# Performance work log

Hardware: AMD Instinct MI355X
Metric: run time of the kernel (lower is better)

The kernel has to match this reference:

```python
import jax, jax.numpy as jnp
import numpy as np

B, N, C = 8, 6000, 21            # batch, proposals (pre_nms_topn), total_labels
VARIANCES = jnp.array([0.1, 0.1, 0.2, 0.2], jnp.float32)
MAX_TOTAL = 200                   # max_total_size == max_output_size_per_class
SCORE_THR = 0.5
IOU_THR = 0.5                     # tf combined_non_max_suppression default
NEG = -1e9                        # finite sentinel for suppressed scores


def setup_inputs() -> dict:
    key = jax.random.key(0)
    k1, k2, k3, k4 = jax.random.split(key, 4)
    # valid normalized rois: y1,x1 in [0,0.8), positive height/width
    yx1 = jax.random.uniform(k1, (B, N, 2), jnp.float32) * 0.8
    hw = jax.random.uniform(k4, (B, N, 2), jnp.float32) * 0.2 + 0.01
    roi_bboxes = jnp.concatenate([yx1, yx1 + hw], axis=-1)  # [B,N,4] y1x1y2x2
    pred_deltas = jax.random.normal(k2, (B, N, C * 4), jnp.float32) * 0.5
    pred_label_probs = jax.random.uniform(k3, (B, N, C), jnp.float32)
    return {"roi_bboxes": roi_bboxes, "pred_deltas": pred_deltas,
            "pred_label_probs": pred_label_probs}


def reference(roi_bboxes, pred_deltas, pred_label_probs):
    # --- bbox delta decoding ---
    deltas = pred_deltas.reshape(B, N, C, 4) * VARIANCES          # [B,N,C,4]
    roi = roi_bboxes[:, :, None, :]                               # [B,N,1,4]
    anc_h = roi[..., 2] - roi[..., 0]
    anc_w = roi[..., 3] - roi[..., 1]
    anc_cy = roi[..., 0] + 0.5 * anc_h
    anc_cx = roi[..., 1] + 0.5 * anc_w
    bh = jnp.exp(deltas[..., 2]) * anc_h
    bw = jnp.exp(deltas[..., 3]) * anc_w
    bcy = deltas[..., 0] * anc_h + anc_cy
    bcx = deltas[..., 1] * anc_w + anc_cx
    y1 = bcy - 0.5 * bh
    x1 = bcx - 0.5 * bw
    y2 = y1 + bh
    x2 = x1 + bw
    boxes = jnp.stack([y1, x1, y2, x2], axis=-1)                  # [B,N,C,4]
    boxes = jnp.clip(boxes, 0.0, 1.0)  # combined NMS clip_boxes=True default

    # zero out scores where argmax class is background (0)
    lbl = jnp.argmax(pred_label_probs, axis=-1)                   # [B,N]
    scores = jnp.where((lbl != 0)[..., None], pred_label_probs, 0.0)

    boxes = boxes.transpose(0, 2, 1, 3)                           # [B,C,N,4]
    scores = scores.transpose(0, 2, 1)                            # [B,C,N]
    s0 = jnp.where(scores > SCORE_THR, scores, NEG)

    areas = (jnp.maximum(boxes[..., 2] - boxes[..., 0], 0.0) *
             jnp.maximum(boxes[..., 3] - boxes[..., 1], 0.0))     # [B,C,N]

    # --- greedy per-class NMS, vectorized over (B,C) ---
    def step(s, _):
        idx = jnp.argmax(s, axis=-1)                              # [B,C]
        val = jnp.take_along_axis(s, idx[..., None], axis=-1)[..., 0]
        box = jnp.take_along_axis(boxes, idx[..., None, None], axis=2)[..., 0, :]
        valid = val > NEG * 0.5
        iy1 = jnp.maximum(box[..., None, 0], boxes[..., 0])
        ix1 = jnp.maximum(box[..., None, 1], boxes[..., 1])
        iy2 = jnp.minimum(box[..., None, 2], boxes[..., 2])
        ix2 = jnp.minimum(box[..., None, 3], boxes[..., 3])
        inter = jnp.maximum(iy2 - iy1, 0.0) * jnp.maximum(ix2 - ix1, 0.0)
        sel_a = (jnp.maximum(box[..., 2] - box[..., 0], 0.0) *
                 jnp.maximum(box[..., 3] - box[..., 1], 0.0))
        iou = inter / (sel_a[..., None] + areas - inter + 1e-8)   # [B,C,N]
        s = jnp.where((iou > IOU_THR) & valid[..., None], NEG, s)
        return s, (box, val, valid)

    _, (sel_box, sel_val, sel_ok) = jax.lax.scan(step, s0, None, length=MAX_TOTAL)
    # [T,B,C,*] -> [B, C*T, *]
    sel_box = sel_box.transpose(1, 2, 0, 3).reshape(B, C * MAX_TOTAL, 4)
    sel_val = sel_val.transpose(1, 2, 0).reshape(B, C * MAX_TOTAL)
    sel_ok = sel_ok.transpose(1, 2, 0).reshape(B, C * MAX_TOTAL)
    cls = jnp.broadcast_to(jnp.arange(C, dtype=jnp.float32)[None, :, None],
                           (B, C, MAX_TOTAL)).reshape(B, C * MAX_TOTAL)

    sel_val = jnp.where(sel_ok, sel_val, NEG)
    top_s, top_i = jax.lax.top_k(sel_val, MAX_TOTAL)              # [B,200]
    fb = jnp.take_along_axis(sel_box, top_i[..., None], axis=1)
    fc = jnp.take_along_axis(cls, top_i, axis=1)
    ok = top_s > NEG * 0.5
    final_scores = jnp.where(ok, top_s, 0.0)
    final_bboxes = jnp.where(ok[..., None], fb, 0.0)
    final_labels = jnp.where(ok, fc, 0.0)
    return final_bboxes, final_labels, final_scores
```

## Files before the change

### kernel.cpp

```cpp
#include <hip/hip_runtime.h>

#define B_    8
#define N_    6000
#define C_    21
#define MAXT  200
#define NEGV  -1000000000.0f
#define UCAP  4096
#define CCAP  1024
#define CTGT  512
#define NBUCK 64
#define NTH   1024
#define NENT  (C_ * MAXT)
#define NBLK  (B_ * C_)


__device__ __forceinline__ unsigned ford(float f) {
  unsigned u = __float_as_uint(f);
  return (u & 0x80000000u) ? ~u : (u | 0x80000000u);
}
__device__ __forceinline__ float funord(unsigned o) {
  unsigned u = (o & 0x80000000u) ? (o ^ 0x80000000u) : ~o;
  return __uint_as_float(u);
}

__device__ __forceinline__ float4 decode_box(const float* __restrict__ roi,
                                             const float* __restrict__ deltas,
                                             int b, int n, int c)
{
#pragma clang fp contract(off)
  float4 r = *(const float4*)(roi + ((size_t)b * N_ + n) * 4);
  float4 d = *(const float4*)(deltas + ((size_t)b * N_ + n) * (C_ * 4) + c * 4);
  float d0 = d.x * 0.1f, d1 = d.y * 0.1f, d2 = d.z * 0.2f, d3 = d.w * 0.2f;
  float ah = r.z - r.x, aw = r.w - r.y;
  float acy = r.x + 0.5f * ah, acx = r.y + 0.5f * aw;
  float bh = expf(d2) * ah, bw = expf(d3) * aw;
  float bcy = d0 * ah + acy, bcx = d1 * aw + acx;
  float y1 = bcy - 0.5f * bh, x1 = bcx - 0.5f * bw;
  float y2 = y1 + bh, x2 = x1 + bw;
  y1 = fminf(fmaxf(y1, 0.f), 1.f); x1 = fminf(fmaxf(x1, 0.f), 1.f);
  y2 = fminf(fmaxf(y2, 0.f), 1.f); x2 = fminf(fmaxf(x2, 0.f), 1.f);
  return make_float4(y1, x1, y2, x2);
}

__device__ __forceinline__ float iou_ref(float4 s, float4 o) {
#pragma clang fp contract(off)
  float iy1 = fmaxf(s.x, o.x), ix1 = fmaxf(s.y, o.y);
  float iy2 = fminf(s.z, o.z), ix2 = fminf(s.w, o.w);
  float inter = fmaxf(iy2 - iy1, 0.f) * fmaxf(ix2 - ix1, 0.f);
  float sa = fmaxf(s.z - s.x, 0.f) * fmaxf(s.w - s.y, 0.f);
  float oa = fmaxf(o.z - o.x, 0.f) * fmaxf(o.w - o.y, 0.f);
  return inter / (sa + oa - inter + 1e-08f);
}

struct Smem {
  unsigned long long ukeys[UCAP];
  unsigned long long cbuf[CCAP];
  float4 cboxAll[512];
  float4 comm[MAXT];
  unsigned long long kill[64];
  unsigned long long s_dead[16];
  int hist[NBUCK];
  int wcnt[16];
  int s_cnt, s_clen, s_ncomm, s_blo, s_len;
};

__global__ __launch_bounds__(256) void prep_kernel(
    const float* __restrict__ probs, float* __restrict__ probsT)
{
  int t = blockIdx.x * 256 + threadIdx.x;
  if (t >= B_ * N_) return;
  int b = t / N_, n = t - b * N_;
  const float* pr = probs + (size_t)t * C_;
  float p[C_];
  #pragma unroll
  for (int k = 0; k < C_; ++k) p[k] = pr[k];
  float mx = p[0]; int am = 0;
  #pragma unroll
  for (int k = 1; k < C_; ++k) { if (p[k] > mx) { mx = p[k]; am = k; } }
  float msk = (am != 0) ? 1.0f : 0.0f;
  #pragma unroll
  for (int c = 0; c < C_; ++c)
    probsT[((size_t)b * C_ + c) * N_ + n] = p[c] * msk;
}

__global__ __launch_bounds__(NTH) void nms_kernel(
    const float* __restrict__ roi, const float* __restrict__ deltas,
    const float* __restrict__ probs, const float* __restrict__ probsT,
    float* __restrict__ sel_val, float* __restrict__ sel_box)
{
#pragma clang fp contract(off)
  __shared__ Smem sm;
  const int bc = blockIdx.x, b = bc / C_, c = bc % C_;
  const int tid = threadIdx.x, lane = tid & 63, wv = tid >> 6;

  if (tid < NBUCK) sm.hist[tid] = 0;
  if (tid == 0) { sm.s_cnt = 0; sm.s_ncomm = 0; }
  __syncthreads();

  int M;
  const float* rowT = probsT ? (probsT + (size_t)bc * N_) : nullptr;
  if (rowT) {
    float scv[6];
    #pragma unroll
    for (int it = 0; it < 6; ++it) {
      int n = it * NTH + tid;
      scv[it] = (n < N_) ? rowT[n] : 0.f;
    }
    int off[6];
    int wtot = 0;
    #pragma unroll
    for (int it = 0; it < 6; ++it) {
      bool cand = (scv[it] > 0.5f);
      unsigned long long m = __ballot(cand);
      off[it] = wtot + __popcll(m & ((1ULL << lane) - 1ULL));
      wtot += __popcll(m);
    }
    if (lane == 0) sm.wcnt[wv] = wtot;
    __syncthreads();
    int wbase = 0, mtot = 0;
    #pragma unroll
    for (int w = 0; w < 16; ++w) {
      int t2 = sm.wcnt[w];
      if (w < wv) wbase += t2;
      mtot += t2;
    }
    #pragma unroll
    for (int it = 0; it < 6; ++it) {
      if (scv[it] > 0.5f) {
        int pos = wbase + off[it];
        if (pos < UCAP) {
          unsigned hi = ford(scv[it]);
          int n = it * NTH + tid;
          sm.ukeys[pos] = ((unsigned long long)hi << 32) |
                          (unsigned)(0xFFFFFFFFu - (unsigned)n);
          atomicAdd(&sm.hist[(hi >> 17) & (NBUCK - 1)], 1);
        }
      }
    }
    __syncthreads();
    M = mtot < UCAP ? mtot : UCAP;
  } else {
    for (int base0 = 0; base0 < N_; base0 += NTH) {
      int n = base0 + tid;
      bool cand = false;
      float sc = 0.f;
      if (n < N_) {
        const float* pr = probs + ((size_t)b * N_ + n) * C_;
        float mx = pr[0]; int am = 0;
        #pragma unroll
        for (int k = 1; k < C_; ++k) { float v = pr[k]; if (v > mx) { mx = v; am = k; } }
        if (am != 0) sc = pr[c];
        cand = (sc > 0.5f);
      }
      unsigned long long m = __ballot(cand);
      int wcnt2 = __popcll(m);
      int bslot = 0;
      if (lane == 0 && wcnt2) bslot = atomicAdd(&sm.s_cnt, wcnt2);
      bslot = __shfl(bslot, 0);
      if (cand) {
        int pos = bslot + __popcll(m & ((1ULL << lane) - 1ULL));
        if (pos < UCAP) {
          unsigned hi = ford(sc);
          sm.ukeys[pos] = ((unsigned long long)hi << 32) |
                          (unsigned)(0xFFFFFFFFu - (unsigned)n);
          atomicAdd(&sm.hist[(hi >> 17) & (NBUCK - 1)], 1);
        }
      }
    }
    __syncthreads();
    M = sm.s_cnt < UCAP ? sm.s_cnt : UCAP;
  }

  float* sv = sel_val + (size_t)bc * MAXT;
  float* sb = sel_box + (size_t)bc * MAXT * 4;

  int bhi = NBUCK - 1;
  while (true) {
    if (sm.s_ncomm >= MAXT || bhi < 0) break;

    if (wv == 0) {
      int h = (lane <= bhi) ? sm.hist[bhi - lane] : 0;
      int p = h;
      #pragma unroll
      for (int d = 1; d < 64; d <<= 1) {
        int o = __shfl_up(p, d);
        if (lane >= d) p += o;
      }
      unsigned long long ok = __ballot(p <= CTGT);
      int m = __popcll(ok);
      if (m == 0) m = 1;
      if (m > bhi + 1) m = bhi + 1;
      int len = __shfl(p, m - 1);
      if (lane == 0) { sm.s_blo = bhi - (m - 1); sm.s_len = len; sm.s_clen = 0; }
    }
    __syncthreads();
    int blo = sm.s_blo;
    if (sm.s_len == 0) break;

    for (int i = tid; i < M; i += NTH) {
      unsigned long long kk = sm.ukeys[i];
      int bk = (int)((kk >> 49) & (NBUCK - 1));
      bool in = (bk >= blo && bk <= bhi);
      unsigned long long mm = __ballot(in);
      int wc = __popcll(mm);
      int bs0 = 0;
      if (lane == 0 && wc) bs0 = atomicAdd(&sm.s_clen, wc);
      bs0 = __shfl(bs0, 0);
      if (in) {
        int p = bs0 + __popcll(mm & ((1ULL << lane) - 1ULL));
        if (p < CCAP) sm.cbuf[p] = kk;
      }
    }
    __syncthreads();
    int alen = sm.s_clen < CCAP ? sm.s_clen : CCAP;

    if (alen > 0) {
      int SORTP = 64;
      while (SORTP < alen) SORTP <<= 1;

      {
        unsigned long long v = (tid < alen) ? sm.cbuf[tid] : 0ULL;
        if (SORTP <= 512) {
          int pb = 0;
          for (int k = 2; k <= SORTP; k <<= 1) {
            for (int j = k >> 1; j > 0; j >>= 1) {
              if (j >= 64) {
                unsigned long long* bf = (pb == 0) ? sm.cbuf : (sm.cbuf + 512);
                pb ^= 1;
                if (tid < SORTP) bf[tid] = v;
                __syncthreads();
                if (tid < SORTP) {
                  unsigned long long w = bf[tid ^ j];
                  bool takeMax = ((tid & j) == 0) == ((tid & k) == 0);
                  if ((w > v) == takeMax) v = w;
                }
              } else if (tid < SORTP) {
                unsigned long long w = __shfl_xor(v, j);
                bool takeMax = ((tid & j) == 0) == ((tid & k) == 0);
                if ((w > v) == takeMax) v = w;
              }
            }
          }
        } else {
          for (int k = 2; k <= SORTP; k <<= 1) {
            for (int j = k >> 1; j > 0; j >>= 1) {
              bool takeMax = ((tid & j) == 0) == ((tid & k) == 0);
              unsigned long long w;
              if (j >= 64) {
                __syncthreads(); sm.cbuf[tid] = v; __syncthreads();
                w = sm.cbuf[tid ^ j];
              } else {
                w = __shfl_xor(v, j);
              }
              if ((w > v) == takeMax) v = w;
            }
          }
        }
        __syncthreads();
        if (tid < SORTP && SORTP <= 512) sm.cbuf[tid] = v;
        else if (SORTP > 512) sm.cbuf[tid] = v;
        __syncthreads();
      }

      if (tid < alen && tid < 512) {
        int n = (int)(0xFFFFFFFFu - (unsigned)(sm.cbuf[tid] & 0xFFFFFFFFull));
        sm.cboxAll[tid] = decode_box(roi, deltas, b, n, c);
      }
      __syncthreads();

      int start = 0;
      int wlen = alen < 512 ? alen : 512;
      while (true) {
        int nc = sm.s_ncomm;
        if (nc >= MAXT || start >= wlen) break;
        int bs = min(64, wlen - start);

        float4 ib = sm.cboxAll[start + lane];
        #pragma unroll
        for (int r = 0; r < 4; ++r) {
          int j = (wv << 2) | r;
          float4 jb4 = sm.cboxAll[start + j];
          bool kf = (j < bs) && (lane < bs) && (lane > j) &&
                    (iou_ref(jb4, ib) > 0.5f);
          unsigned long long rowm = __ballot(kf);
          if (lane == 0) sm.kill[j] = rowm;
        }
        {
          bool dead = false;
          if (lane < bs) {
            for (int jc = wv; jc < nc; jc += 16) {
              if (iou_ref(sm.comm[jc], ib) > 0.5f) { dead = true; break; }
            }
          }
          unsigned long long dm = __ballot(dead);
          if (lane == 0) sm.s_dead[wv] = dm;
        }
        __syncthreads();

        if (wv == 0) {
          unsigned long long sup = sm.s_dead[0];
          #pragma unroll
          for (int w2 = 1; w2 < 16; ++w2) sup |= sm.s_dead[w2];
          unsigned long long row = sm.kill[lane];
          #pragma unroll
          for (int s5 = 0; s5 < 6; ++s5) {
            const unsigned long long Ms[6] = {
              0x5555555555555555ULL, 0x3333333333333333ULL,
              0x0F0F0F0F0F0F0F0FULL, 0x00FF00FF00FF00FFULL,
              0x0000FFFF0000FFFFULL, 0x00000000FFFFFFFFULL };
            int d = 1 << s5;
            unsigned long long other = __shfl_xor(row, d);
            unsigned long long Mk = Ms[s5];
            row = ((lane & d) == 0) ? ((row & Mk) | ((other & Mk) << d))
                                    : ((row & ~Mk) | ((other & ~Mk) >> d));
          }
          unsigned long long col = row;

          unsigned long long alive = ~sup;
          if (bs < 64) alive &= (1ULL << bs) - 1ULL;
          unsigned long long pend = alive, chosen = 0ULL;
          while (pend) {
            bool rdy_b = ((col & pend) == 0ULL);
            unsigned long long rdy = __ballot(rdy_b) & pend;
            bool kld_b = ((col & chosen) != 0ULL);
            unsigned long long kl = __ballot(kld_b);
            chosen |= rdy & ~kl;
            pend &= ~rdy;
          }
          int take = MAXT - nc;
          if (__popcll(chosen) > take) {
            bool keep = ((chosen >> lane) & 1ULL) &&
                        (__popcll(chosen & ((1ULL << lane) - 1ULL)) < take);
            chosen = __ballot(keep);
          }
          if ((chosen >> lane) & 1ULL) {
            int rnk = nc + __popcll(chosen & ((1ULL << lane) - 1ULL));
            float4 bb2 = sm.cboxAll[start + lane];
            sm.comm[rnk] = bb2;
            sv[rnk] = funord((unsigned)(sm.cbuf[start + lane] >> 32));
            sb[(size_t)rnk * 4 + 0] = bb2.x; sb[(size_t)rnk * 4 + 1] = bb2.y;
            sb[(size_t)rnk * 4 + 2] = bb2.z; sb[(size_t)rnk * 4 + 3] = bb2.w;
          }
          if (lane == 0) sm.s_ncomm = nc + __popcll(chosen);
        }
        __syncthreads();
        start += bs;
      }
    }
    bhi = blo - 1;
  }

  int T = sm.s_ncomm;
  for (int j2 = T + tid; j2 < MAXT; j2 += NTH) sv[j2] = NEGV;
}

__global__ __launch_bounds__(NTH) void merge2_kernel(
    const float* __restrict__ sel_val, const float* __restrict__ sel_box,
    float* __restrict__ out)
{
  __shared__ Smem sm;
  const int bc = blockIdx.x;
  const int b = bc / C_, sc = bc % C_;
  const int tid = threadIdx.x;
  int* s_rank = reinterpret_cast<int*>(sm.cboxAll);

  for (int i = tid; i < NENT; i += NTH) {
    float v = sel_val[(size_t)b * NENT + i];
    unsigned long long key = ((unsigned long long)ford(v) << 32) |
                             (unsigned)(0xFFFFFFFFu - (unsigned)i);
    if (i < UCAP) sm.ukeys[i] = key; else sm.cbuf[i - UCAP] = key;
  }
  if (tid < MAXT) s_rank[tid] = 0;
  __syncthreads();

  auto klds = [&](int i) -> unsigned long long {
    return (i < UCAP) ? sm.ukeys[i] : sm.cbuf[i - UCAP];
  };

  if (tid < 1000) {
    int q = tid / MAXT, t = tid - q * MAXT;
    int e = sc * MAXT + t;
    unsigned long long mykey = klds(e);
    int part = 0;
    for (int cc = q; cc < C_; cc += 5) {
      int lo = 0, hi = MAXT;
      while (lo < hi) {
        int mid = (lo + hi) >> 1;
        if (klds(cc * MAXT + mid) > mykey) lo = mid + 1; else hi = mid;
      }
      part += lo;
    }
    atomicAdd(&s_rank[t], part);
  }
  __syncthreads();

  if (tid < MAXT) {
    int t = tid;
    int e = sc * MAXT + t;
    int rank = s_rank[t];
    if (rank < MAXT) {
      float* obx = out + (size_t)b * MAXT * 4;
      float* olb = out + (size_t)B_ * MAXT * 4 + (size_t)b * MAXT;
      float* osc = out + (size_t)B_ * MAXT * 5 + (size_t)b * MAXT;
      float v = funord((unsigned)(klds(e) >> 32));
      if (v > NEGV * 0.5f) {
        osc[rank] = v;
        olb[rank] = (float)sc;
        const float* bp = sel_box + ((size_t)b * NENT + e) * 4;
        obx[rank * 4 + 0] = bp[0]; obx[rank * 4 + 1] = bp[1];
        obx[rank * 4 + 2] = bp[2]; obx[rank * 4 + 3] = bp[3];
      } else {
        osc[rank] = 0.f; olb[rank] = 0.f;
        obx[rank * 4 + 0] = 0.f; obx[rank * 4 + 1] = 0.f;
        obx[rank * 4 + 2] = 0.f; obx[rank * 4 + 3] = 0.f;
      }
    }
  }
}

extern "C" void kernel_launch(void* const* d_in, const int* in_sizes, int n_in,
                              void* d_out, int out_size, void* d_ws, size_t ws_size,
                              hipStream_t stream)
{
  const float* roi    = (const float*)d_in[0];
  const float* deltas = (const float*)d_in[1];
  const float* probs  = (const float*)d_in[2];
  float* out = (float*)d_out;
  float* ws  = (float*)d_ws;

  float* sel_val = ws;
  float* sel_box = ws + (size_t)B_ * NENT;
  float* probsT  = ws + (size_t)B_ * NENT * 5;
  size_t need_mid = ((size_t)B_ * NENT * 5 + (size_t)B_ * C_ * N_) * sizeof(float);
  bool haveT = (ws_size >= need_mid);

  const float* probsT_arg = haveT ? probsT : nullptr;
  if (haveT)
    prep_kernel<<<dim3((B_ * N_ + 255) / 256), dim3(256), 0, stream>>>(probs, probsT);
  nms_kernel<<<dim3(NBLK), dim3(NTH), 0, stream>>>(
      roi, deltas, probs, probsT_arg, sel_val, sel_box);
  merge2_kernel<<<dim3(NBLK), dim3(NTH), 0, stream>>>(sel_val, sel_box, out);
}
```

Baseline: 102.5 us.

## Scatter candidates into per-bucket slots and sort each bucket within a wave

```diff
diff --git a/kernel.cpp b/kernel.cpp
--- a/kernel.cpp
+++ b/kernel.cpp
@@ -60,8 +60,9 @@
   unsigned long long kill[64];
   unsigned long long s_dead[16];
   int hist[NBUCK];
+  int ctr[NBUCK];
   int wcnt[16];
-  int s_cnt, s_clen, s_ncomm, s_blo, s_len;
+  int s_cnt, s_clen, s_ncomm, s_blo, s_len, s_m, s_mx;
 };
 
 __global__ __launch_bounds__(256) void prep_kernel(
@@ -191,74 +192,96 @@
       if (m == 0) m = 1;
       if (m > bhi + 1) m = bhi + 1;
       int len = __shfl(p, m - 1);
-      if (lane == 0) { sm.s_blo = bhi - (m - 1); sm.s_len = len; sm.s_clen = 0; }
+      if (lane < m) sm.ctr[bhi - lane] = p - h;
+      int hv = (lane < m) ? h : 0;
+      #pragma unroll
+      for (int d = 1; d < 64; d <<= 1) hv = max(hv, __shfl_xor(hv, d));
+      if (lane == 0) {
+        sm.s_blo = bhi - (m - 1); sm.s_len = len; sm.s_clen = 0;
+        sm.s_m = m; sm.s_mx = hv;
+      }
     }
     __syncthreads();
     int blo = sm.s_blo;
     if (sm.s_len == 0) break;
+    int mbk = sm.s_m, mxb = sm.s_mx;
 
     for (int i = tid; i < M; i += NTH) {
       unsigned long long kk = sm.ukeys[i];
       int bk = (int)((kk >> 49) & (NBUCK - 1));
-      bool in = (bk >= blo && bk <= bhi);
-      unsigned long long mm = __ballot(in);
-      int wc = __popcll(mm);
-      int bs0 = 0;
-      if (lane == 0 && wc) bs0 = atomicAdd(&sm.s_clen, wc);
-      bs0 = __shfl(bs0, 0);
-      if (in) {
-        int p = bs0 + __popcll(mm & ((1ULL << lane) - 1ULL));
-        if (p < CCAP) sm.cbuf[p] = kk;
+      if (bk >= blo && bk <= bhi) {
+        int slot = atomicAdd(&sm.ctr[bk], 1);
+        if (slot < CCAP) sm.cbuf[slot] = kk;
       }
     }
     __syncthreads();
-    int alen = sm.s_clen < CCAP ? sm.s_clen : CCAP;
+    int alen = sm.s_len < CCAP ? sm.s_len : CCAP;
 
     if (alen > 0) {
-      int SORTP = 64;
-      while (SORTP < alen) SORTP <<= 1;
-
-      {
-        unsigned long long v = (tid < alen) ? sm.cbuf[tid] : 0ULL;
-        if (SORTP <= 512) {
-          int pb = 0;
-          for (int k = 2; k <= SORTP; k <<= 1) {
-            for (int j = k >> 1; j > 0; j >>= 1) {
-              if (j >= 64) {
-                unsigned long long* bf = (pb == 0) ? sm.cbuf : (sm.cbuf + 512);
-                pb ^= 1;
-                if (tid < SORTP) bf[tid] = v;
-                __syncthreads();
-                if (tid < SORTP) {
-                  unsigned long long w = bf[tid ^ j];
-                  bool takeMax = ((tid & j) == 0) == ((tid & k) == 0);
-                  if ((w > v) == takeMax) v = w;
-                }
-              } else if (tid < SORTP) {
-                unsigned long long w = __shfl_xor(v, j);
-                bool takeMax = ((tid & j) == 0) == ((tid & k) == 0);
+      if (alen <= 512 && mxb <= 128) {
+        for (int j = wv; j < mbk; j += 16) {
+          int bk = bhi - j;
+          int len = sm.hist[bk];
+          if (len <= 0) continue;
+          int base = sm.ctr[bk] - len;
+          if (len <= 64) {
+            unsigned long long v = (lane < len) ? sm.cbuf[base + lane] : 0ULL;
+            #pragma unroll
+            for (int k = 2; k <= 64; k <<= 1) {
+              for (int jj = k >> 1; jj > 0; jj >>= 1) {
+                unsigned long long w = __shfl_xor(v, jj);
+                bool takeMax = ((lane & jj) == 0) == ((lane & k) == 0);
                 if ((w > v) == takeMax) v = w;
               }
             }
-          }
-        } else {
-          for (int k = 2; k <= SORTP; k <<= 1) {
-            for (int j = k >> 1; j > 0; j >>= 1) {
-              bool takeMax = ((tid & j) == 0) == ((tid & k) == 0);
-              unsigned long long w;
-              if (j >= 64) {
-                __syncthreads(); sm.cbuf[tid] = v; __syncthreads();
-                w = sm.cbuf[tid ^ j];
-              } else {
-                w = __shfl_xor(v, j);
+            if (lane < len) sm.cbuf[base + lane] = v;
+          } else {
+            unsigned long long v0 = (lane < len) ? sm.cbuf[base + lane] : 0ULL;
+            unsigned long long v1 = (64 + lane < len) ? sm.cbuf[base + 64 + lane] : 0ULL;
+            #pragma unroll
+            for (int k = 2; k <= 128; k <<= 1) {
+              for (int jj = k >> 1; jj > 0; jj >>= 1) {
+                if (jj == 64) {
+                  unsigned long long a = (v0 > v1) ? v0 : v1;
+                  unsigned long long bmin = (v0 > v1) ? v1 : v0;
+                  v0 = a; v1 = bmin;
+                } else {
+                  unsigned long long w0 = __shfl_xor(v0, jj);
+                  unsigned long long w1 = __shfl_xor(v1, jj);
+                  bool e0k = ((lane & k) == 0);
+                  bool e1k = (((lane + 64) & k) == 0);
+                  bool jz = ((lane & jj) == 0);
+                  bool tm0 = (jz == e0k);
+                  bool tm1 = (jz == e1k);
+                  if ((w0 > v0) == tm0) v0 = w0;
+                  if ((w1 > v1) == tm1) v1 = w1;
+                }
               }
-              if ((w > v) == takeMax) v = w;
             }
+            if (lane < len) sm.cbuf[base + lane] = v0;
+            if (64 + lane < len) sm.cbuf[base + 64 + lane] = v1;
           }
         }
         __syncthreads();
-        if (tid < SORTP && SORTP <= 512) sm.cbuf[tid] = v;
-        else if (SORTP > 512) sm.cbuf[tid] = v;
+      } else {
+        int SORTP = 64;
+        while (SORTP < alen) SORTP <<= 1;
+        unsigned long long v = (tid < alen) ? sm.cbuf[tid] : 0ULL;
+        for (int k = 2; k <= SORTP; k <<= 1) {
+          for (int j = k >> 1; j > 0; j >>= 1) {
+            bool takeMax = ((tid & j) == 0) == ((tid & k) == 0);
+            unsigned long long w;
+            if (j >= 64) {
+              __syncthreads(); if (tid < SORTP) sm.cbuf[tid] = v; __syncthreads();
+              w = sm.cbuf[tid ^ j];
+            } else {
+              w = __shfl_xor(v, j);
+            }
+            if (tid < SORTP && (w > v) == takeMax) v = w;
+          }
+        }
+        __syncthreads();
+        if (tid < SORTP) sm.cbuf[tid] = v;
         __syncthreads();
       }
 
```

New measurement: 97.51 us. 1.05x faster.
